# Kernel optimization log

Hardware: AMD Instinct MI355X
Metric: run time of the kernel (lower is better)

Reference implementation:

```python
import jax, jax.numpy as jnp
import numpy as np

B, N, D = 8, 10000, 16
E = 320000
EH, EOUT, NOUT = 32, 30, 64

def setup_inputs() -> dict:
    key = jax.random.key(0)
    ks = jax.random.split(key, 12)
    x = jax.random.normal(ks[0], (B, N, D), dtype=jnp.float32)
    edge_index = jax.random.randint(ks[1], (2, E), 0, N, dtype=jnp.int32)
    # edge_attr: col 0 = city distance (keep away from 0), col 1 = direction
    dist = jax.random.uniform(ks[2], (E,), dtype=jnp.float32) * 100.0 + 1.0
    direc = jax.random.uniform(ks[3], (E,), dtype=jnp.float32) * 360.0
    edge_attr = jnp.stack([dist, direc], axis=-1)
    wind_mean = jnp.array([3.0, 180.0], dtype=jnp.float32)
    wind_std = jnp.array([1.5, 90.0], dtype=jnp.float32)
    W1 = jax.random.normal(ks[4], (2 * D + 2 + 1, EH), dtype=jnp.float32) * 0.1
    b1 = jnp.zeros((EH,), dtype=jnp.float32)
    W2 = jax.random.normal(ks[5], (EH, EOUT), dtype=jnp.float32) * 0.1
    b2 = jnp.zeros((EOUT,), dtype=jnp.float32)
    Wn = jax.random.normal(ks[6], (EOUT, NOUT), dtype=jnp.float32) * 0.1
    bn = jnp.zeros((NOUT,), dtype=jnp.float32)
    return {"x": x, "edge_index": edge_index, "edge_attr": edge_attr,
            "wind_mean": wind_mean, "wind_std": wind_std,
            "W1": W1, "b1": b1, "W2": W2, "b2": b2, "Wn": Wn, "bn": bn}

def reference(x, edge_index, edge_attr, wind_mean, wind_std, W1, b1, W2, b2, Wn, bn):
    src, tgt = edge_index[0], edge_index[1]
    node_src = x[:, src]      # [B, E, D]
    node_tgt = x[:, tgt]      # [B, E, D]
    # de-normalize wind features (last 2 channels)
    src_wind = node_src[:, :, -2:] * wind_std[None, None, :] + wind_mean[None, None, :]
    speed = src_wind[:, :, 0]
    direc = src_wind[:, :, 1]
    city_dist = edge_attr[:, 0][None, :]   # [1, E]
    city_direc = edge_attr[:, 1][None, :]
    theta = jnp.abs(city_direc - direc)
    edge_weight = jax.nn.relu(3.0 * speed * jnp.cos(theta) / city_dist)  # [B, E]
    # normalized edge attributes (torch std is unbiased)
    ea_norm = (edge_attr - edge_attr.mean(axis=0)) / jnp.std(edge_attr, axis=0, ddof=1)
    ea_norm_b = jnp.broadcast_to(ea_norm[None, :, :], (x.shape[0], ea_norm.shape[0], 2))
    feat = jnp.concatenate([node_src, node_tgt, ea_norm_b, edge_weight[:, :, None]], axis=-1)  # [B, E, 2D+3]
    h = jax.nn.sigmoid(feat @ W1 + b1)
    e = jax.nn.sigmoid(h @ W2 + b2)        # [B, E, EOUT]
    agg = jnp.zeros((x.shape[0], x.shape[1], e.shape[-1]), dtype=e.dtype)
    agg = agg.at[:, tgt].add(e)
    agg = agg.at[:, src].add(-e)
    out = jax.nn.sigmoid(agg @ Wn + bn)    # [B, N, NOUT]
    return out
```

## Files before the change

kernel.cpp:

```cpp
#include <hip/hip_runtime.h>
#include <hip/hip_bf16.h>
#include <math.h>

#define B 8
#define N 10000
#define D 16
#define E 320000
#define EH 32
#define EOUT 30
#define NOUT 64
#define FEAT 35
#define FILL_BLOCKS ((E + 255) / 256)
#define PQ_BLOCKS   ((B * N * 64) / 256)

typedef short bf16x8 __attribute__((ext_vector_type(8)));
typedef float f32x4 __attribute__((ext_vector_type(4)));

#define LDS_FENCE() asm volatile("" ::: "memory")

__device__ __forceinline__ float sigmoidf_(float v) {
    return __builtin_amdgcn_rcpf(1.0f + __expf(-v));
}

__device__ __forceinline__ unsigned int pack_bf16_2(float a, float b) {
    unsigned ua = __float_as_uint(a), ub = __float_as_uint(b);
    ua = (ua + 0x7FFFu + ((ua >> 16) & 1u)) >> 16;
    ub = (ub + 0x7FFFu + ((ub >> 16) & 1u)) >> 16;
    return ua | (ub << 16);
}

__device__ __forceinline__ unsigned short bf16rn(float f) {
    unsigned u = __float_as_uint(f);
    u = (u + 0x7FFFu + ((u >> 16) & 1u)) >> 16;
    return (unsigned short)u;
}

__global__ void __launch_bounds__(256) stats_pq_kernel(
    const float* __restrict__ ea, const int* __restrict__ eidx,
    float* __restrict__ stats, int* __restrict__ cnt,
    const float* __restrict__ x, const float* __restrict__ W1,
    const float* __restrict__ b1,
    unsigned short* __restrict__ Pb, unsigned short* __restrict__ Qb)
{
    if (blockIdx.x < 256) {
        float s0 = 0.f, s1 = 0.f, q0 = 0.f, q1 = 0.f;
        for (int i = blockIdx.x * 256 + threadIdx.x; i < E; i += 256 * 256) {
            float2 v = *(const float2*)(ea + 2 * (size_t)i);
            s0 += v.x; q0 += v.x * v.x;
            s1 += v.y; q1 += v.y * v.y;
            atomicAdd(&cnt[eidx[E + i]], 1);
            atomicAdd(&cnt[N + eidx[i]], 1);
        }
        #pragma unroll
        for (int off = 32; off > 0; off >>= 1) {
            s0 += __shfl_down(s0, off);
            s1 += __shfl_down(s1, off);
            q0 += __shfl_down(q0, off);
            q1 += __shfl_down(q1, off);
        }
        if ((threadIdx.x & 63) == 0) {
            atomicAdd(&stats[0], s0);
            atomicAdd(&stats[1], s1);
            atomicAdd(&stats[2], q0);
            atomicAdd(&stats[3], q1);
        }
    } else {
        int wid = ((blockIdx.x - 256) * 256 + threadIdx.x) >> 6;
        int lane = threadIdx.x & 63;
        if (wid >= B * N) return;
        int j = lane & 31;
        int half = lane >> 5;
        const float* xr = x + (size_t)wid * D;
        float acc = half ? b1[j] : 0.f;
        const float* Wb = W1 + (half ? D * EH : 0);
        #pragma unroll
        for (int d = 0; d < D; d++)
            acc = fmaf(xr[d], Wb[d * EH + j], acc);
        float accN = __shfl_down(acc, 1);
        if (!(lane & 1)) {
            unsigned u = pack_bf16_2(acc, accN);
            unsigned short* dst = (half ? Qb : Pb) + (size_t)wid * EH + j;
            *(unsigned*)dst = u;
        }
    }
}

__global__ void stats_count_kernel(const float* __restrict__ ea,
                                   const int* __restrict__ eidx,
                                   float* __restrict__ stats,
                                   int* __restrict__ cnt) {
    float s0 = 0.f, s1 = 0.f, q0 = 0.f, q1 = 0.f;
    for (int i = blockIdx.x * blockDim.x + threadIdx.x; i < E; i += gridDim.x * blockDim.x) {
        float2 v = *(const float2*)(ea + 2 * (size_t)i);
        s0 += v.x; q0 += v.x * v.x;
        s1 += v.y; q1 += v.y * v.y;
        atomicAdd(&cnt[eidx[E + i]], 1);
        atomicAdd(&cnt[N + eidx[i]], 1);
    }
    #pragma unroll
    for (int off = 32; off > 0; off >>= 1) {
        s0 += __shfl_down(s0, off);
        s1 += __shfl_down(s1, off);
        q0 += __shfl_down(q0, off);
        q1 += __shfl_down(q1, off);
    }
    if ((threadIdx.x & 63) == 0) {
        atomicAdd(&stats[0], s0);
        atomicAdd(&stats[1], s1);
        atomicAdd(&stats[2], q0);
        atomicAdd(&stats[3], q1);
    }
}

__global__ void __launch_bounds__(1024) scan_kernel(const int* __restrict__ cnt_in,
                                                    int* __restrict__ offs,
                                                    int* __restrict__ cursor,
                                                    float* __restrict__ stats,
                                                    const float* __restrict__ W2,
                                                    unsigned short* __restrict__ w2f) {
    if (threadIdx.x == 0) {
        const float n = (float)E;
        float s0 = stats[0], s1 = stats[1], q0 = stats[2], q1 = stats[3];
        float v0 = (q0 - s0 * s0 / n) / (n - 1.0f);
        float v1 = (q1 - s1 * s1 / n) / (n - 1.0f);
        stats[4] = s0 / n;
        stats[5] = 1.0f / sqrtf(v0);
        stats[6] = s1 / n;
        stats[7] = 1.0f / sqrtf(v1);
    }
    if (threadIdx.x < 128) {
        int tl = threadIdx.x >> 6;
        int ln = threadIdx.x & 63;
        int k0 = (ln >> 4) * 8;
        int col = tl * 16 + (ln & 15);
        unsigned short* hi = w2f + ((size_t)(tl * 2 + 0) * 64 + ln) * 8;
        unsigned short* lo = w2f + ((size_t)(tl * 2 + 1) * 64 + ln) * 8;
        #pragma unroll
        for (int j = 0; j < 8; j++) {
            float w = (col < EOUT) ? W2[(k0 + j) * EOUT + col] : 0.0f;
            unsigned u = __float_as_uint(w) & 0xFFFF0000u;
            float r = w - __uint_as_float(u);
            hi[j] = (unsigned short)(u >> 16);
            lo[j] = bf16rn(r);
        }
    }
    const int M = 2 * N;
    const int CH = 20;
    __shared__ int lds[1024];
    int t = threadIdx.x;
    int base = t * CH;
    int loc[CH];
    int s = 0;
    #pragma unroll
    for (int i = 0; i < CH; i++) {
        int idx = base + i;
        int v = (idx < M) ? cnt_in[idx] : 0;
        loc[i] = s;
        s += v;
    }
    lds[t] = s;
    __syncthreads();
    for (int off = 1; off < 1024; off <<= 1) {
        int v = (t >= off) ? lds[t - off] : 0;
        __syncthreads();
        lds[t] += v;
        __syncthreads();
    }
    int tbase = (t > 0) ? lds[t - 1] : 0;
    #pragma unroll
    for (int i = 0; i < CH; i++) {
        int idx = base + i;
        if (idx < M) {
            offs[idx] = tbase + loc[i];
            cursor[idx] = tbase + loc[i];
        }
    }
    if (t == 1023) offs[M] = lds[1023];
}

__global__ void __launch_bounds__(256) edge_mlp_kernel(
    const float* __restrict__ x, const int* __restrict__ eidx,
    const float* __restrict__ ea,
    const float* __restrict__ wind_mean, const float* __restrict__ wind_std,
    const float* __restrict__ W1, const float* __restrict__ b2,
    const float* __restrict__ stats,
    const unsigned short* __restrict__ Pb, const unsigned short* __restrict__ Qb,
    const unsigned short* __restrict__ w2f,
    unsigned short* __restrict__ eBuf,
    int* __restrict__ cursor, int* __restrict__ lists,
    int b0, int period)
{
    __shared__ unsigned short hsh[4][64][64];

    int bid = blockIdx.x;
    if (period) {
        int k = bid / period;
        int r = bid - k * period;
        if (r == period - 1) {
            int e = k * 256 + threadIdx.x;
            if (e < E) {
                int p = atomicAdd(&cursor[eidx[E + e]], 1);
                lists[p] = e;
                int q = atomicAdd(&cursor[N + eidx[e]], 1);
                lists[q] = e;
            }
            return;
        }
        bid -= k;
    }

    int t = bid * 256 + threadIdx.x;
    int bb = t / E;
    int e = t - bb * E;
    int b = b0 + bb;
    int wv = threadIdx.x >> 6;
    int lane = threadIdx.x & 63;

    int src = eidx[e];
    int tgt = eidx[E + e];

    const uint4* Pr = (const uint4*)(Pb + ((size_t)b * N + src) * EH);
    const uint4* Qr = (const uint4*)(Qb + ((size_t)b * N + tgt) * EH);

    float h[EH];
    #pragma unroll
    for (int i = 0; i < 4; i++) {
        uint4 p = Pr[i];
        uint4 q = Qr[i];
        unsigned pu[4] = {p.x, p.y, p.z, p.w};
        unsigned qu[4] = {q.x, q.y, q.z, q.w};
        #pragma unroll
        for (int k2 = 0; k2 < 4; k2++) {
            float pl = __uint_as_float(pu[k2] << 16);
            float ph = __uint_as_float(pu[k2] & 0xFFFF0000u);
            float ql = __uint_as_float(qu[k2] << 16);
            float qh = __uint_as_float(qu[k2] & 0xFFFF0000u);
            h[8 * i + 2 * k2 + 0] = pl + ql;
            h[8 * i + 2 * k2 + 1] = ph + qh;
        }
    }

    float2 eav = *(const float2*)(ea + 2 * (size_t)e);
    float dist = eav.x, cdir = eav.y;
    float f32v = (dist - stats[4]) * stats[5];
    float f33v = (cdir - stats[6]) * stats[7];

    float2 xw = *(const float2*)(x + ((size_t)b * N + src) * D + 14);
    float speed = xw.x * wind_std[0] + wind_mean[0];
    float sdir  = xw.y * wind_std[1] + wind_mean[1];
    float ew = fmaxf(3.0f * speed * __cosf(fabsf(cdir - sdir)) *
                     __builtin_amdgcn_rcpf(dist), 0.0f);

    const float* W1r32 = W1 + 32 * EH;
    const float* W1r33 = W1 + 33 * EH;
    const float* W1r34 = W1 + 34 * EH;
    #pragma unroll
    for (int j = 0; j < EH; j++) {
        float v = h[j];
        v = fmaf(f32v, W1r32[j], v);
        v = fmaf(f33v, W1r33[j], v);
        v = fmaf(ew,   W1r34[j], v);
        h[j] = sigmoidf_(v);
    }

    unsigned short* myrow = &hsh[wv][lane][0];
    int lx = lane & 7;
    #pragma unroll
    for (int i = 0; i < 4; i++) {
        unsigned hw[4];
        #pragma unroll
        for (int p = 0; p < 4; p++)
            hw[p] = pack_bf16_2(h[8 * i + 2 * p], h[8 * i + 2 * p + 1]);
        *(uint4*)(myrow + ((i ^ lx) << 3)) = make_uint4(hw[0], hw[1], hw[2], hw[3]);
    }
    LDS_FENCE();

    union { uint4 u; bf16x8 v; } bf[4];
    const uint4* wfp = (const uint4*)w2f;
    #pragma unroll
    for (int i = 0; i < 4; i++) bf[i].u = wfp[i * 64 + lane];

    int m  = lane & 15;
    int hr = lane >> 4;
    float bias0 = b2[m];
    float bias1 = (m < EOUT - 16) ? b2[16 + m] : 0.0f;

    f32x4 acc[4][2];
    #pragma unroll
    for (int g = 0; g < 4; g++) {
        f32x4 z0 = {bias0, bias0, bias0, bias0};
        f32x4 z1 = {bias1, bias1, bias1, bias1};
        acc[g][0] = z0;
        acc[g][1] = z1;
    }

    int mx = m & 7;
    #pragma unroll
    for (int g = 0; g < 4; g++) {
        const unsigned short* rp = &hsh[wv][g * 16 + m][0];
        bf16x8 Ah = *(const bf16x8*)(rp + ((hr ^ mx) << 3));
        acc[g][0] = __builtin_amdgcn_mfma_f32_16x16x32_bf16(Ah, bf[0].v, acc[g][0], 0, 0, 0);
        acc[g][1] = __builtin_amdgcn_mfma_f32_16x16x32_bf16(Ah, bf[2].v, acc[g][1], 0, 0, 0);
        acc[g][0] = __builtin_amdgcn_mfma_f32_16x16x32_bf16(Ah, bf[1].v, acc[g][0], 0, 0, 0);
        acc[g][1] = __builtin_amdgcn_mfma_f32_16x16x32_bf16(Ah, bf[3].v, acc[g][1], 0, 0, 0);
    }
    LDS_FENCE();

    unsigned short* wb = &hsh[wv][0][0];
    int c0 = m >> 3;
    int c1 = 2 + (m >> 3);
    int mp = m & 7;
    #pragma unroll
    for (int g = 0; g < 4; g++) {
        #pragma unroll
        for (int j = 0; j < 4; j++) {
            int er  = g * 16 + hr * 4 + j;
            int swz = ((hr & 1) << 2) | j;
            float v0 = sigmoidf_(acc[g][0][j]);
            float v1 = sigmoidf_(acc[g][1][j]);
            wb[er * 64 + ((c0 ^ swz) << 3) + mp] = bf16rn(v0);
            wb[er * 64 + ((c1 ^ swz) << 3) + mp] =
                (m < 14) ? bf16rn(v1) : (unsigned short)0;
        }
    }
    LDS_FENCE();

    int eWaveBase = e - lane;
    int rrow = lane >> 2;
    int rx   = rrow & 7;
    unsigned short* wdst = eBuf + ((size_t)bb * E + eWaveBase) * EH;
    #pragma unroll
    for (int i = 0; i < 4; i++) {
        uint4 v = *(const uint4*)(wb + (i * 16 + rrow) * 64 + (((lane & 3) ^ rx) << 3));
        *(uint4*)(wdst + i * 512 + lane * 8) = v;
    }
}

__global__ void __launch_bounds__(256) gather_kernel(
    const unsigned short* __restrict__ eBuf, const int* __restrict__ offs,
    const int* __restrict__ lists, const float* __restrict__ Wn,
    const float* __restrict__ bn, float* __restrict__ out, int b0, int nb)
{
    int wid = (blockIdx.x * blockDim.x + threadIdx.x) >> 6;
    int lane = threadIdx.x & 63;
    if (wid >= nb * N) return;
    int bb = wid / N;
    int node = wid - bb * N;
    int b = b0 + bb;

    int g = lane >> 2;
    int c = lane & 3;
    const uint4* ebase = (const uint4*)(eBuf + (size_t)bb * E * EH);

    float a0 = 0.f, a1 = 0.f, a2 = 0.f, a3 = 0.f;
    float a4 = 0.f, a5 = 0.f, a6 = 0.f, a7 = 0.f;

    {
        int s = offs[node], e1 = offs[node + 1];
        for (int r = s; r < e1; r += 16) {
            int row = r + g;
            if (row < e1) {
                int eid = lists[row];
                uint4 v = ebase[(size_t)eid * 4 + c];
                a0 += __uint_as_float(v.x << 16);
                a1 += __uint_as_float(v.x & 0xFFFF0000u);
                a2 += __uint_as_float(v.y << 16);
                a3 += __uint_as_float(v.y & 0xFFFF0000u);
                a4 += __uint_as_float(v.z << 16);
                a5 += __uint_as_float(v.z & 0xFFFF0000u);
                a6 += __uint_as_float(v.w << 16);
                a7 += __uint_as_float(v.w & 0xFFFF0000u);
            }
        }
    }
    {
        int s = offs[N + node], e1 = offs[N + node + 1];
        for (int r = s; r < e1; r += 16) {
            int row = r + g;
            if (row < e1) {
                int eid = lists[row];
                uint4 v = ebase[(size_t)eid * 4 + c];
                a0 -= __uint_as_float(v.x << 16);
                a1 -= __uint_as_float(v.x & 0xFFFF0000u);
                a2 -= __uint_as_float(v.y << 16);
                a3 -= __uint_as_float(v.y & 0xFFFF0000u);
                a4 -= __uint_as_float(v.z << 16);
                a5 -= __uint_as_float(v.z & 0xFFFF0000u);
                a6 -= __uint_as_float(v.w << 16);
                a7 -= __uint_as_float(v.w & 0xFFFF0000u);
            }
        }
    }

    #pragma unroll
    for (int off = 4; off <= 32; off <<= 1) {
        a0 += __shfl_xor(a0, off); a1 += __shfl_xor(a1, off);
        a2 += __shfl_xor(a2, off); a3 += __shfl_xor(a3, off);
        a4 += __shfl_xor(a4, off); a5 += __shfl_xor(a5, off);
        a6 += __shfl_xor(a6, off); a7 += __shfl_xor(a7, off);
    }

    float o = bn[lane];
    #pragma unroll
    for (int k = 0; k < EOUT; k++) {
        float av;
        switch (k & 7) {
            case 0:  av = a0; break;
            case 1:  av = a1; break;
            case 2:  av = a2; break;
            case 3:  av = a3; break;
            case 4:  av = a4; break;
            case 5:  av = a5; break;
            case 6:  av = a6; break;
            default: av = a7; break;
        }
        float ak = __shfl(av, k >> 3);
        o = fmaf(ak, Wn[k * NOUT + lane], o);
    }
    out[((size_t)b * N + node) * NOUT + lane] = sigmoidf_(o);
}

__global__ void __launch_bounds__(256) edge_kernel_atomic(
    const float* __restrict__ x, const int* __restrict__ eidx,
    const float* __restrict__ ea,
    const float* __restrict__ wind_mean, const float* __restrict__ wind_std,
    const float* __restrict__ W1, const float* __restrict__ b1,
    const float* __restrict__ W2, const float* __restrict__ b2,
    const float* __restrict__ stats, float* __restrict__ agg)
{
    int t = blockIdx.x * blockDim.x + threadIdx.x;
    if (t >= B * E) return;
    int b = t / E;
    int e = t - b * E;
    int src = eidx[e];
    int tgt = eidx[E + e];
    const float* xs = x + ((size_t)b * N + src) * D;
    const float* xt = x + ((size_t)b * N + tgt) * D;
    float f[FEAT];
    #pragma unroll
    for (int i = 0; i < D; i++) f[i] = xs[i];
    #pragma unroll
    for (int i = 0; i < D; i++) f[D + i] = xt[i];
    float2 eav = *(const float2*)(ea + 2 * (size_t)e);
    f[32] = (eav.x - stats[4]) * stats[5];
    f[33] = (eav.y - stats[6]) * stats[7];
    float speed = f[14] * wind_std[0] + wind_mean[0];
    float sdir  = f[15] * wind_std[1] + wind_mean[1];
    f[34] = fmaxf(3.0f * speed * cosf(fabsf(eav.y - sdir)) / eav.x, 0.0f);
    float h[EH];
    #pragma unroll
    for (int j = 0; j < EH; j++) h[j] = b1[j];
    #pragma unroll
    for (int k = 0; k < FEAT; k++) {
        float fk = f[k];
        #pragma unroll
        for (int j = 0; j < EH; j++) h[j] = fmaf(fk, W1[k * EH + j], h[j]);
    }
    #pragma unroll
    for (int j = 0; j < EH; j++) h[j] = sigmoidf_(h[j]);
    float o[EOUT];
    #pragma unroll
    for (int j = 0; j < EOUT; j++) o[j] = b2[j];
    #pragma unroll
    for (int k = 0; k < EH; k++) {
        float hk = h[k];
        #pragma unroll
        for (int j = 0; j < EOUT; j++) o[j] = fmaf(hk, W2[k * EOUT + j], o[j]);
    }
    float* at = agg + ((size_t)b * N + tgt) * EOUT;
    float* as = agg + ((size_t)b * N + src) * EOUT;
    #pragma unroll
    for (int j = 0; j < EOUT; j++) {
        float v = sigmoidf_(o[j]);
        atomicAdd(at + j,  v);
        atomicAdd(as + j, -v);
    }
}

__global__ void __launch_bounds__(256) node_kernel_fallback(
    const float* __restrict__ agg, const float* __restrict__ Wn,
    const float* __restrict__ bn, float* __restrict__ out)
{
    int t = blockIdx.x * blockDim.x + threadIdx.x;
    if (t >= B * N * NOUT) return;
    int row = t >> 6;
    int j   = t & 63;
    const float* a = agg + (size_t)row * EOUT;
    float acc = bn[j];
    #pragma unroll
    for (int k = 0; k < EOUT; k++) acc = fmaf(a[k], Wn[k * NOUT + j], acc);
    out[t] = sigmoidf_(acc);
}

extern "C" void kernel_launch(void* const* d_in, const int* in_sizes, int n_in,
                              void* d_out, int out_size, void* d_ws, size_t ws_size,
                              hipStream_t stream) {
    const float* x         = (const float*)d_in[0];
    const int*   eidx      = (const int*)d_in[1];
    const float* ea        = (const float*)d_in[2];
    const float* wind_mean = (const float*)d_in[3];
    const float* wind_std  = (const float*)d_in[4];
    const float* W1        = (const float*)d_in[5];
    const float* b1        = (const float*)d_in[6];
    const float* W2        = (const float*)d_in[7];
    const float* b2        = (const float*)d_in[8];
    const float* Wn        = (const float*)d_in[9];
    const float* bn        = (const float*)d_in[10];
    float* out = (float*)d_out;

    char* ws = (char*)d_ws;
    float*          stats = (float*)(ws + 0);
    unsigned short* w2f   = (unsigned short*)(ws + 256);
    int*            offs  = (int*)(ws + 4352);
    int*            cnt   = (int*)(ws + 84480);
    int*            lists = (int*)(ws + 164608);
    unsigned short* Pb    = (unsigned short*)(ws + 2724608);
    unsigned short* Qb    = (unsigned short*)(ws + 7844608);
    unsigned short* eBuf  = (unsigned short*)(ws + 12964608);
    const size_t fixed = 12964608;
    const size_t perBatch = (size_t)E * EH * sizeof(unsigned short);

    if (ws_size >= fixed + perBatch) {
        int chunk = (int)((ws_size - fixed) / perBatch);
        if (chunk > 8) chunk = 8;

        hipMemsetAsync(ws, 0, 164608, stream);

        stats_pq_kernel<<<256 + PQ_BLOCKS, 256, 0, stream>>>(
            ea, eidx, stats, cnt, x, W1, b1, Pb, Qb);
        scan_kernel<<<1, 1024, 0, stream>>>(cnt, offs, cnt, stats, W2, w2f);

        for (int b0 = 0; b0 < B; b0 += chunk) {
            int nb = B - b0; if (nb > chunk) nb = chunk;
            int eblk = nb * E / 256;
            int period = (b0 == 0) ? (nb + 1) : 0;
            int grid = eblk + ((b0 == 0) ? FILL_BLOCKS : 0);
            edge_mlp_kernel<<<grid, 256, 0, stream>>>(
                x, eidx, ea, wind_mean, wind_std, W1, b2, stats,
                Pb, Qb, w2f, eBuf, cnt, lists, b0, period);
            gather_kernel<<<nb * (N * 64 / 256), 256, 0, stream>>>(
                eBuf, offs, lists, Wn, bn, out, b0, nb);
        }
    } else {
        float* agg = (float*)(ws + 164608);
        size_t zero_bytes = 164608 + (size_t)B * N * EOUT * sizeof(float);
        hipMemsetAsync(ws, 0, zero_bytes, stream);
        stats_count_kernel<<<256, 256, 0, stream>>>(ea, eidx, stats, cnt);
        scan_kernel<<<1, 1024, 0, stream>>>(cnt, offs, cnt, stats, W2, w2f);
        int nwork = B * E;
        edge_kernel_atomic<<<(nwork + 255) / 256, 256, 0, stream>>>(
            x, eidx, ea, wind_mean, wind_std, W1, b1, W2, b2, stats, agg);
        int nout_elems = B * N * NOUT;
        node_kernel_fallback<<<(nout_elems + 255) / 256, 256, 0, stream>>>(
            agg, Wn, bn, out);
    }
}
```

Baseline: 368.1 us.

## Interleave gather of first batch half with edge MLP of second half

The Pb/Qb projection moves out of the stats kernel and into the single-block scan kernel as extra 1024-thread blocks. When all eight batches fit in the workspace, edge MLP work is split into two halves. The second launch interleaves edge-MLP blocks for batches 4-7 with gather blocks for batches 0-3 in a 1:2 ratio, and a final gather handles batches 4-7. The aim is to overlap the bandwidth-heavy gather with compute-heavy MFMA work and cut tail effects, at the cost of an extra launch and more complex block scheduling.

```diff
diff --git a/kernel.cpp b/kernel.cpp
--- a/kernel.cpp
+++ b/kernel.cpp
@@ -11,7 +11,7 @@
 #define NOUT 64
 #define FEAT 35
 #define FILL_BLOCKS ((E + 255) / 256)
-#define PQ_BLOCKS   ((B * N * 64) / 256)
+#define PQ1K_BLOCKS ((B * N) / 16)
 
 typedef short bf16x8 __attribute__((ext_vector_type(8)));
 typedef float f32x4 __attribute__((ext_vector_type(4)));
@@ -35,37 +35,43 @@
     return (unsigned short)u;
 }
 
-__global__ void __launch_bounds__(256) stats_pq_kernel(
+__global__ void __launch_bounds__(256) stats_count_kernel(
     const float* __restrict__ ea, const int* __restrict__ eidx,
-    float* __restrict__ stats, int* __restrict__ cnt,
+    float* __restrict__ stats, int* __restrict__ cnt)
+{
+    float s0 = 0.f, s1 = 0.f, q0 = 0.f, q1 = 0.f;
+    for (int i = blockIdx.x * blockDim.x + threadIdx.x; i < E; i += gridDim.x * blockDim.x) {
+        float2 v = *(const float2*)(ea + 2 * (size_t)i);
+        s0 += v.x; q0 += v.x * v.x;
+        s1 += v.y; q1 += v.y * v.y;
+        atomicAdd(&cnt[eidx[E + i]], 1);
+        atomicAdd(&cnt[N + eidx[i]], 1);
+    }
+    #pragma unroll
+    for (int off = 32; off > 0; off >>= 1) {
+        s0 += __shfl_down(s0, off);
+        s1 += __shfl_down(s1, off);
+        q0 += __shfl_down(q0, off);
+        q1 += __shfl_down(q1, off);
+    }
+    if ((threadIdx.x & 63) == 0) {
+        atomicAdd(&stats[0], s0);
+        atomicAdd(&stats[1], s1);
+        atomicAdd(&stats[2], q0);
+        atomicAdd(&stats[3], q1);
+    }
+}
+
+__global__ void __launch_bounds__(1024) scan_pq_kernel(
+    const int* __restrict__ cnt_in, int* __restrict__ offs,
+    int* __restrict__ cursor, float* __restrict__ stats,
+    const float* __restrict__ W2, unsigned short* __restrict__ w2f,
     const float* __restrict__ x, const float* __restrict__ W1,
     const float* __restrict__ b1,
     unsigned short* __restrict__ Pb, unsigned short* __restrict__ Qb)
 {
-    if (blockIdx.x < 256) {
-        float s0 = 0.f, s1 = 0.f, q0 = 0.f, q1 = 0.f;
-        for (int i = blockIdx.x * 256 + threadIdx.x; i < E; i += 256 * 256) {
-            float2 v = *(const float2*)(ea + 2 * (size_t)i);
-            s0 += v.x; q0 += v.x * v.x;
-            s1 += v.y; q1 += v.y * v.y;
-            atomicAdd(&cnt[eidx[E + i]], 1);
-            atomicAdd(&cnt[N + eidx[i]], 1);
-        }
-        #pragma unroll
-        for (int off = 32; off > 0; off >>= 1) {
-            s0 += __shfl_down(s0, off);
-            s1 += __shfl_down(s1, off);
-            q0 += __shfl_down(q0, off);
-            q1 += __shfl_down(q1, off);
-        }
-        if ((threadIdx.x & 63) == 0) {
-            atomicAdd(&stats[0], s0);
-            atomicAdd(&stats[1], s1);
-            atomicAdd(&stats[2], q0);
-            atomicAdd(&stats[3], q1);
-        }
-    } else {
-        int wid = ((blockIdx.x - 256) * 256 + threadIdx.x) >> 6;
+    if (blockIdx.x > 0) {
+        int wid = (blockIdx.x - 1) * 16 + (threadIdx.x >> 6);
         int lane = threadIdx.x & 63;
         if (wid >= B * N) return;
         int j = lane & 31;
@@ -82,42 +88,9 @@
             unsigned short* dst = (half ? Qb : Pb) + (size_t)wid * EH + j;
             *(unsigned*)dst = u;
         }
-    }
-}
-
-__global__ void stats_count_kernel(const float* __restrict__ ea,
-                                   const int* __restrict__ eidx,
-                                   float* __restrict__ stats,
-                                   int* __restrict__ cnt) {
-    float s0 = 0.f, s1 = 0.f, q0 = 0.f, q1 = 0.f;
-    for (int i = blockIdx.x * blockDim.x + threadIdx.x; i < E; i += gridDim.x * blockDim.x) {
-        float2 v = *(const float2*)(ea + 2 * (size_t)i);
-        s0 += v.x; q0 += v.x * v.x;
-        s1 += v.y; q1 += v.y * v.y;
-        atomicAdd(&cnt[eidx[E + i]], 1);
-        atomicAdd(&cnt[N + eidx[i]], 1);
-    }
-    #pragma unroll
-    for (int off = 32; off > 0; off >>= 1) {
-        s0 += __shfl_down(s0, off);
-        s1 += __shfl_down(s1, off);
-        q0 += __shfl_down(q0, off);
-        q1 += __shfl_down(q1, off);
-    }
-    if ((threadIdx.x & 63) == 0) {
-        atomicAdd(&stats[0], s0);
-        atomicAdd(&stats[1], s1);
-        atomicAdd(&stats[2], q0);
-        atomicAdd(&stats[3], q1);
-    }
-}
-
-__global__ void __launch_bounds__(1024) scan_kernel(const int* __restrict__ cnt_in,
-                                                    int* __restrict__ offs,
-                                                    int* __restrict__ cursor,
-                                                    float* __restrict__ stats,
-                                                    const float* __restrict__ W2,
-                                                    unsigned short* __restrict__ w2f) {
+        return;
+    }
+
     if (threadIdx.x == 0) {
         const float n = (float)E;
         float s0 = stats[0], s1 = stats[1], q0 = stats[2], q1 = stats[3];
@@ -178,179 +151,22 @@
     if (t == 1023) offs[M] = lds[1023];
 }
 
-__global__ void __launch_bounds__(256) edge_mlp_kernel(
-    const float* __restrict__ x, const int* __restrict__ eidx,
-    const float* __restrict__ ea,
-    const float* __restrict__ wind_mean, const float* __restrict__ wind_std,
-    const float* __restrict__ W1, const float* __restrict__ b2,
-    const float* __restrict__ stats,
-    const unsigned short* __restrict__ Pb, const unsigned short* __restrict__ Qb,
-    const unsigned short* __restrict__ w2f,
-    unsigned short* __restrict__ eBuf,
-    int* __restrict__ cursor, int* __restrict__ lists,
-    int b0, int period)
-{
-    __shared__ unsigned short hsh[4][64][64];
-
-    int bid = blockIdx.x;
-    if (period) {
-        int k = bid / period;
-        int r = bid - k * period;
-        if (r == period - 1) {
-            int e = k * 256 + threadIdx.x;
-            if (e < E) {
-                int p = atomicAdd(&cursor[eidx[E + e]], 1);
-                lists[p] = e;
-                int q = atomicAdd(&cursor[N + eidx[e]], 1);
-                lists[q] = e;
-            }
-            return;
-        }
-        bid -= k;
-    }
-
-    int t = bid * 256 + threadIdx.x;
-    int bb = t / E;
-    int e = t - bb * E;
-    int b = b0 + bb;
-    int wv = threadIdx.x >> 6;
-    int lane = threadIdx.x & 63;
-
-    int src = eidx[e];
-    int tgt = eidx[E + e];
-
-    const uint4* Pr = (const uint4*)(Pb + ((size_t)b * N + src) * EH);
-    const uint4* Qr = (const uint4*)(Qb + ((size_t)b * N + tgt) * EH);
-
-    float h[EH];
-    #pragma unroll
-    for (int i = 0; i < 4; i++) {
-        uint4 p = Pr[i];
-        uint4 q = Qr[i];
-        unsigned pu[4] = {p.x, p.y, p.z, p.w};
-        unsigned qu[4] = {q.x, q.y, q.z, q.w};
-        #pragma unroll
-        for (int k2 = 0; k2 < 4; k2++) {
-            float pl = __uint_as_float(pu[k2] << 16);
-            float ph = __uint_as_float(pu[k2] & 0xFFFF0000u);
-            float ql = __uint_as_float(qu[k2] << 16);
-            float qh = __uint_as_float(qu[k2] & 0xFFFF0000u);
-            h[8 * i + 2 * k2 + 0] = pl + ql;
-            h[8 * i + 2 * k2 + 1] = ph + qh;
-        }
-    }
-
-    float2 eav = *(const float2*)(ea + 2 * (size_t)e);
-    float dist = eav.x, cdir = eav.y;
-    float f32v = (dist - stats[4]) * stats[5];
-    float f33v = (cdir - stats[6]) * stats[7];
-
-    float2 xw = *(const float2*)(x + ((size_t)b * N + src) * D + 14);
-    float speed = xw.x * wind_std[0] + wind_mean[0];
-    float sdir  = xw.y * wind_std[1] + wind_mean[1];
-    float ew = fmaxf(3.0f * speed * __cosf(fabsf(cdir - sdir)) *
-                     __builtin_amdgcn_rcpf(dist), 0.0f);
-
-    const float* W1r32 = W1 + 32 * EH;
-    const float* W1r33 = W1 + 33 * EH;
-    const float* W1r34 = W1 + 34 * EH;
-    #pragma unroll
-    for (int j = 0; j < EH; j++) {
-        float v = h[j];
-        v = fmaf(f32v, W1r32[j], v);
-        v = fmaf(f33v, W1r33[j], v);
-        v = fmaf(ew,   W1r34[j], v);
-        h[j] = sigmoidf_(v);
-    }
-
-    unsigned short* myrow = &hsh[wv][lane][0];
-    int lx = lane & 7;
-    #pragma unroll
-    for (int i = 0; i < 4; i++) {
-        unsigned hw[4];
-        #pragma unroll
-        for (int p = 0; p < 4; p++)
-            hw[p] = pack_bf16_2(h[8 * i + 2 * p], h[8 * i + 2 * p + 1]);
-        *(uint4*)(myrow + ((i ^ lx) << 3)) = make_uint4(hw[0], hw[1], hw[2], hw[3]);
-    }
-    LDS_FENCE();
-
-    union { uint4 u; bf16x8 v; } bf[4];
-    const uint4* wfp = (const uint4*)w2f;
-    #pragma unroll
-    for (int i = 0; i < 4; i++) bf[i].u = wfp[i * 64 + lane];
-
-    int m  = lane & 15;
-    int hr = lane >> 4;
-    float bias0 = b2[m];
-    float bias1 = (m < EOUT - 16) ? b2[16 + m] : 0.0f;
-
-    f32x4 acc[4][2];
-    #pragma unroll
-    for (int g = 0; g < 4; g++) {
-        f32x4 z0 = {bias0, bias0, bias0, bias0};
-        f32x4 z1 = {bias1, bias1, bias1, bias1};
-        acc[g][0] = z0;
-        acc[g][1] = z1;
-    }
-
-    int mx = m & 7;
-    #pragma unroll
-    for (int g = 0; g < 4; g++) {
-        const unsigned short* rp = &hsh[wv][g * 16 + m][0];
-        bf16x8 Ah = *(const bf16x8*)(rp + ((hr ^ mx) << 3));
-        acc[g][0] = __builtin_amdgcn_mfma_f32_16x16x32_bf16(Ah, bf[0].v, acc[g][0], 0, 0, 0);
-        acc[g][1] = __builtin_amdgcn_mfma_f32_16x16x32_bf16(Ah, bf[2].v, acc[g][1], 0, 0, 0);
-        acc[g][0] = __builtin_amdgcn_mfma_f32_16x16x32_bf16(Ah, bf[1].v, acc[g][0], 0, 0, 0);
-        acc[g][1] = __builtin_amdgcn_mfma_f32_16x16x32_bf16(Ah, bf[3].v, acc[g][1], 0, 0, 0);
-    }
-    LDS_FENCE();
-
-    unsigned short* wb = &hsh[wv][0][0];
-    int c0 = m >> 3;
-    int c1 = 2 + (m >> 3);
-    int mp = m & 7;
-    #pragma unroll
-    for (int g = 0; g < 4; g++) {
-        #pragma unroll
-        for (int j = 0; j < 4; j++) {
-            int er  = g * 16 + hr * 4 + j;
-            int swz = ((hr & 1) << 2) | j;
-            float v0 = sigmoidf_(acc[g][0][j]);
-            float v1 = sigmoidf_(acc[g][1][j]);
-            wb[er * 64 + ((c0 ^ swz) << 3) + mp] = bf16rn(v0);
-            wb[er * 64 + ((c1 ^ swz) << 3) + mp] =
-                (m < 14) ? bf16rn(v1) : (unsigned short)0;
-        }
-    }
-    LDS_FENCE();
-
-    int eWaveBase = e - lane;
-    int rrow = lane >> 2;
-    int rx   = rrow & 7;
-    unsigned short* wdst = eBuf + ((size_t)bb * E + eWaveBase) * EH;
-    #pragma unroll
-    for (int i = 0; i < 4; i++) {
-        uint4 v = *(const uint4*)(wb + (i * 16 + rrow) * 64 + (((lane & 3) ^ rx) << 3));
-        *(uint4*)(wdst + i * 512 + lane * 8) = v;
-    }
-}
-
-__global__ void __launch_bounds__(256) gather_kernel(
+__device__ __forceinline__ void gather_node(
+    int gk, int b0, int nbg, int ebOff,
     const unsigned short* __restrict__ eBuf, const int* __restrict__ offs,
     const int* __restrict__ lists, const float* __restrict__ Wn,
-    const float* __restrict__ bn, float* __restrict__ out, int b0, int nb)
-{
-    int wid = (blockIdx.x * blockDim.x + threadIdx.x) >> 6;
+    const float* __restrict__ bn, float* __restrict__ out)
+{
+    int wid = gk * 4 + (threadIdx.x >> 6);
     int lane = threadIdx.x & 63;
-    if (wid >= nb * N) return;
+    if (wid >= nbg * N) return;
     int bb = wid / N;
     int node = wid - bb * N;
     int b = b0 + bb;
 
     int g = lane >> 2;
     int c = lane & 3;
-    const uint4* ebase = (const uint4*)(eBuf + (size_t)bb * E * EH);
+    const uint4* ebase = (const uint4*)(eBuf + (size_t)(b - ebOff) * E * EH);
 
     float a0 = 0.f, a1 = 0.f, a2 = 0.f, a3 = 0.f;
     float a4 = 0.f, a5 = 0.f, a6 = 0.f, a7 = 0.f;
@@ -420,6 +236,184 @@
     out[((size_t)b * N + node) * NOUT + lane] = sigmoidf_(o);
 }
 
+__global__ void __launch_bounds__(256) gather_kernel(
+    const unsigned short* __restrict__ eBuf, const int* __restrict__ offs,
+    const int* __restrict__ lists, const float* __restrict__ Wn,
+    const float* __restrict__ bn, float* __restrict__ out,
+    int b0, int nb, int ebOff)
+{
+    gather_node(blockIdx.x, b0, nb, ebOff, eBuf, offs, lists, Wn, bn, out);
+}
+
+__global__ void __launch_bounds__(256) edge_mlp_kernel(
+    const float* __restrict__ x, const int* __restrict__ eidx,
+    const float* __restrict__ ea,
+    const float* __restrict__ wind_mean, const float* __restrict__ wind_std,
+    const float* __restrict__ W1, const float* __restrict__ b2,
+    const float* __restrict__ stats,
+    const unsigned short* __restrict__ Pb, const unsigned short* __restrict__ Qb,
+    const unsigned short* __restrict__ w2f,
+    unsigned short* __restrict__ eBuf,
+    int* __restrict__ cursor, int* __restrict__ lists,
+    const int* __restrict__ offs, const float* __restrict__ Wn,
+    const float* __restrict__ bn, float* __restrict__ out,
+    int b0, int period, int gmix, int b0g, int nbg, int ebOff)
+{
+    __shared__ unsigned short hsh[4][64][64];
+
+    int bid = blockIdx.x;
+    if (gmix) {
+        int k = bid / 3;
+        int r = bid - k * 3;
+        if (r) {
+            gather_node(2 * k + r - 1, b0g, nbg, ebOff,
+                        eBuf, offs, lists, Wn, bn, out);
+            return;
+        }
+        bid = k;
+    } else if (period) {
+        int k = bid / period;
+        int r = bid - k * period;
+        if (r == period - 1) {
+            int e = k * 256 + threadIdx.x;
+            if (e < E) {
+                int p = atomicAdd(&cursor[eidx[E + e]], 1);
+                lists[p] = e;
+                int q = atomicAdd(&cursor[N + eidx[e]], 1);
+                lists[q] = e;
+            }
+            return;
+        }
+        bid -= k;
+    }
+
+    int t = bid * 256 + threadIdx.x;
+    int bb = t / E;
+    int e = t - bb * E;
+    int b = b0 + bb;
+    int wv = threadIdx.x >> 6;
+    int lane = threadIdx.x & 63;
+
+    int src = eidx[e];
+    int tgt = eidx[E + e];
+
+    const uint4* Pr = (const uint4*)(Pb + ((size_t)b * N + src) * EH);
+    const uint4* Qr = (const uint4*)(Qb + ((size_t)b * N + tgt) * EH);
+
+    float h[EH];
+    #pragma unroll
+    for (int i = 0; i < 4; i++) {
+        uint4 p = Pr[i];
+        uint4 q = Qr[i];
+        unsigned pu[4] = {p.x, p.y, p.z, p.w};
+        unsigned qu[4] = {q.x, q.y, q.z, q.w};
+        #pragma unroll
+        for (int k2 = 0; k2 < 4; k2++) {
+            float pl = __uint_as_float(pu[k2] << 16);
+            float ph = __uint_as_float(pu[k2] & 0xFFFF0000u);
+            float ql = __uint_as_float(qu[k2] << 16);
+            float qh = __uint_as_float(qu[k2] & 0xFFFF0000u);
+            h[8 * i + 2 * k2 + 0] = pl + ql;
+            h[8 * i + 2 * k2 + 1] = ph + qh;
+        }
+    }
+
+    float2 eav = *(const float2*)(ea + 2 * (size_t)e);
+    float dist = eav.x, cdir = eav.y;
+    float f32v = (dist - stats[4]) * stats[5];
+    float f33v = (cdir - stats[6]) * stats[7];
+
+    float2 xw = *(const float2*)(x + ((size_t)b * N + src) * D + 14);
+    float speed = xw.x * wind_std[0] + wind_mean[0];
+    float sdir  = xw.y * wind_std[1] + wind_mean[1];
+    float ew = fmaxf(3.0f * speed * __cosf(fabsf(cdir - sdir)) *
+                     __builtin_amdgcn_rcpf(dist), 0.0f);
+
+    const float* W1r32 = W1 + 32 * EH;
+    const float* W1r33 = W1 + 33 * EH;
+    const float* W1r34 = W1 + 34 * EH;
+    #pragma unroll
+    for (int j = 0; j < EH; j++) {
+        float v = h[j];
+        v = fmaf(f32v, W1r32[j], v);
+        v = fmaf(f33v, W1r33[j], v);
+        v = fmaf(ew,   W1r34[j], v);
+        h[j] = sigmoidf_(v);
+    }
+
+    unsigned short* myrow = &hsh[wv][lane][0];
+    int lx = lane & 7;
+    #pragma unroll
+    for (int i = 0; i < 4; i++) {
+        unsigned hw[4];
+        #pragma unroll
+        for (int p = 0; p < 4; p++)
+            hw[p] = pack_bf16_2(h[8 * i + 2 * p], h[8 * i + 2 * p + 1]);
+        *(uint4*)(myrow + ((i ^ lx) << 3)) = make_uint4(hw[0], hw[1], hw[2], hw[3]);
+    }
+    LDS_FENCE();
+
+    union { uint4 u; bf16x8 v; } bf[4];
+    const uint4* wfp = (const uint4*)w2f;
+    #pragma unroll
+    for (int i = 0; i < 4; i++) bf[i].u = wfp[i * 64 + lane];
+
+    int m  = lane & 15;
+    int hr = lane >> 4;
+    float bias0 = b2[m];
+    float bias1 = (m < EOUT - 16) ? b2[16 + m] : 0.0f;
+
+    f32x4 acc[4][2];
+    #pragma unroll
+    for (int g = 0; g < 4; g++) {
+        f32x4 z0 = {bias0, bias0, bias0, bias0};
+        f32x4 z1 = {bias1, bias1, bias1, bias1};
+        acc[g][0] = z0;
+        acc[g][1] = z1;
+    }
+
+    int mx = m & 7;
+    #pragma unroll
+    for (int g = 0; g < 4; g++) {
+        const unsigned short* rp = &hsh[wv][g * 16 + m][0];
+        bf16x8 Ah = *(const bf16x8*)(rp + ((hr ^ mx) << 3));
+        acc[g][0] = __builtin_amdgcn_mfma_f32_16x16x32_bf16(Ah, bf[0].v, acc[g][0], 0, 0, 0);
+        acc[g][1] = __builtin_amdgcn_mfma_f32_16x16x32_bf16(Ah, bf[2].v, acc[g][1], 0, 0, 0);
+        acc[g][0] = __builtin_amdgcn_mfma_f32_16x16x32_bf16(Ah, bf[1].v, acc[g][0], 0, 0, 0);
+        acc[g][1] = __builtin_amdgcn_mfma_f32_16x16x32_bf16(Ah, bf[3].v, acc[g][1], 0, 0, 0);
+    }
+    LDS_FENCE();
+
+    unsigned short* wb = &hsh[wv][0][0];
+    int c0 = m >> 3;
+    int c1 = 2 + (m >> 3);
+    int mp = m & 7;
+    #pragma unroll
+    for (int g = 0; g < 4; g++) {
+        #pragma unroll
+        for (int j = 0; j < 4; j++) {
+            int er  = g * 16 + hr * 4 + j;
+            int swz = ((hr & 1) << 2) | j;
+            float v0 = sigmoidf_(acc[g][0][j]);
+            float v1 = sigmoidf_(acc[g][1][j]);
+            wb[er * 64 + ((c0 ^ swz) << 3) + mp] = bf16rn(v0);
+            wb[er * 64 + ((c1 ^ swz) << 3) + mp] =
+                (m < 14) ? bf16rn(v1) : (unsigned short)0;
+        }
+    }
+    LDS_FENCE();
+
+    int eWaveBase = e - lane;
+    int rrow = lane >> 2;
+    int rx   = rrow & 7;
+    unsigned short* wdst = eBuf + ((size_t)(b - ebOff) * E + eWaveBase) * EH;
+    #pragma unroll
+    for (int i = 0; i < 4; i++) {
+        uint4 v = *(const uint4*)(wb + (i * 16 + rrow) * 64 + (((lane & 3) ^ rx) << 3));
+        *(uint4*)(wdst + i * 512 + lane * 8) = v;
+    }
+}
+
 __global__ void __launch_bounds__(256) edge_kernel_atomic(
     const float* __restrict__ x, const int* __restrict__ eidx,
     const float* __restrict__ ea,
@@ -526,27 +520,43 @@
 
         hipMemsetAsync(ws, 0, 164608, stream);
 
-        stats_pq_kernel<<<256 + PQ_BLOCKS, 256, 0, stream>>>(
-            ea, eidx, stats, cnt, x, W1, b1, Pb, Qb);
-        scan_kernel<<<1, 1024, 0, stream>>>(cnt, offs, cnt, stats, W2, w2f);
-
-        for (int b0 = 0; b0 < B; b0 += chunk) {
-            int nb = B - b0; if (nb > chunk) nb = chunk;
-            int eblk = nb * E / 256;
-            int period = (b0 == 0) ? (nb + 1) : 0;
-            int grid = eblk + ((b0 == 0) ? FILL_BLOCKS : 0);
-            edge_mlp_kernel<<<grid, 256, 0, stream>>>(
+        stats_count_kernel<<<256, 256, 0, stream>>>(ea, eidx, stats, cnt);
+        scan_pq_kernel<<<1 + PQ1K_BLOCKS, 1024, 0, stream>>>(
+            cnt, offs, cnt, stats, W2, w2f, x, W1, b1, Pb, Qb);
+
+        if (chunk >= 8) {
+            edge_mlp_kernel<<<4 * 1250 + FILL_BLOCKS, 256, 0, stream>>>(
                 x, eidx, ea, wind_mean, wind_std, W1, b2, stats,
-                Pb, Qb, w2f, eBuf, cnt, lists, b0, period);
-            gather_kernel<<<nb * (N * 64 / 256), 256, 0, stream>>>(
-                eBuf, offs, lists, Wn, bn, out, b0, nb);
+                Pb, Qb, w2f, eBuf, cnt, lists, offs, Wn, bn, out,
+                0, 5, 0, 0, 0, 0);
+            edge_mlp_kernel<<<4 * 1250 * 3, 256, 0, stream>>>(
+                x, eidx, ea, wind_mean, wind_std, W1, b2, stats,
+                Pb, Qb, w2f, eBuf, cnt, lists, offs, Wn, bn, out,
+                4, 0, 1, 0, 4, 0);
+            gather_kernel<<<4 * (N / 4), 256, 0, stream>>>(
+                eBuf, offs, lists, Wn, bn, out, 4, 4, 0);
+        } else {
+            for (int b0 = 0; b0 < B; b0 += chunk) {
+                int nb = B - b0; if (nb > chunk) nb = chunk;
+                int eblk = nb * E / 256;
+                int period = (b0 == 0) ? (nb + 1) : 0;
+                int grid = eblk + ((b0 == 0) ? FILL_BLOCKS : 0);
+                edge_mlp_kernel<<<grid, 256, 0, stream>>>(
+                    x, eidx, ea, wind_mean, wind_std, W1, b2, stats,
+                    Pb, Qb, w2f, eBuf, cnt, lists, offs, Wn, bn, out,
+                    b0, period, 0, 0, 0, b0);
+                gather_kernel<<<nb * (N / 4), 256, 0, stream>>>(
+                    eBuf, offs, lists, Wn, bn, out, b0, nb, b0);
+            }
         }
     } else {
         float* agg = (float*)(ws + 164608);
         size_t zero_bytes = 164608 + (size_t)B * N * EOUT * sizeof(float);
         hipMemsetAsync(ws, 0, zero_bytes, stream);
         stats_count_kernel<<<256, 256, 0, stream>>>(ea, eidx, stats, cnt);
-        scan_kernel<<<1, 1024, 0, stream>>>(cnt, offs, cnt, stats, W2, w2f);
+        scan_pq_kernel<<<1, 1024, 0, stream>>>(
+            cnt, offs, cnt, stats, W2, w2f, x, W1, b1,
+            (unsigned short*)(ws + 256), (unsigned short*)(ws + 256));
         int nwork = B * E;
         edge_kernel_atomic<<<(nwork + 255) / 256, 256, 0, stream>>>(
             x, eidx, ea, wind_mean, wind_std, W1, b1, W2, b2, stats, agg);
```

New measurement: 382.3 us. 1.04x slower.
